# Optimization experiments

Hardware: AMD Instinct MI355X
Metric: run time of the kernel (lower is better)

## Reference

```python
import jax, jax.numpy as jnp
import numpy as np

N_NODES = 50000
N_EDGES = 100000
N_RELS = 64
D_IN = 64
D_OUT = 64


def setup_inputs() -> dict:
    key = jax.random.key(0)
    k1, k2, k3, k4, k5, k6 = jax.random.split(key, 6)
    h = jax.random.normal(k1, (N_NODES, D_IN), dtype=jnp.float32)
    src = jax.random.randint(k2, (N_EDGES,), 0, N_NODES)
    rel = jax.random.randint(k3, (N_EDGES,), 0, N_RELS)
    dst = jax.random.randint(k4, (N_EDGES,), 0, N_NODES)
    edges = jnp.stack([src, rel, dst], axis=1)
    # xavier_uniform with gain for relu: bound = gain * sqrt(6 / (fan_in + fan_out))
    gain = float(np.sqrt(2.0))
    bound = gain * float(np.sqrt(6.0 / (D_IN + D_OUT)))
    weight = jax.random.uniform(k5, (N_RELS, D_IN, D_OUT), dtype=jnp.float32,
                                minval=-bound, maxval=bound)
    self_loop_weight = jax.random.uniform(k6, (D_IN, D_OUT), dtype=jnp.float32,
                                          minval=-bound, maxval=bound)
    return {"h": h, "edges": edges, "weight": weight,
            "self_loop_weight": self_loop_weight}


def reference(h, edges, weight, self_loop_weight):
    # h: (N, D_IN); edges: (E, 3) int columns (src, rel, dst)
    src, rel, dst = edges[:, 0], edges[:, 1], edges[:, 2]
    n_nodes = h.shape[0]
    n_edges = src.shape[0]

    # per-edge relation-specific transform: (E,1,in) bmm (E,in,out) -> (E,out)
    src_h = h[src]                                    # (E, D_IN)
    msg = jnp.einsum('ei,eio->eo', src_h, weight[rel])  # (E, D_OUT)

    # -> last edge index per destination node
    last_edge = jax.ops.segment_max(jnp.arange(n_edges, dtype=jnp.int32), dst,
                                    num_segments=n_nodes)  # (N,)
    # msg = msg[index_matrix[dst]]: every edge to node d takes the msg of the
    # last edge pointing to d
    msg = msg[last_edge[dst]]                          # (E, D_OUT)

    # scatter-mean aggregate over dst (only nodes with incoming edges updated)
    sums = jax.ops.segment_sum(msg, dst, num_segments=n_nodes)          # (N, D_OUT)
    counts = jax.ops.segment_sum(jnp.ones((n_edges,), h.dtype), dst,
                                 num_segments=n_nodes)                   # (N,)
    has_in = counts > 0
    agg = jnp.where(has_in[:, None],
                    sums / jnp.maximum(counts, 1.0)[:, None], 0.0)

    out = h @ self_loop_weight                         # (N, D_OUT)
    return out + agg
```

## Files before the change

kernel.cpp:

```cpp
#include <hip/hip_runtime.h>

#define NN 50000
#define NE 100000
#define NREL 64
#define D 64
#define RCAP 1280
#define SCAP 8192
#define CSTR 16
#define BR   8
#define SBLK 64
#define FILL_BLOCKS 128
#define FILL_ITERS  2

typedef unsigned long long u64;
using f16x8 = __attribute__((ext_vector_type(8))) _Float16;
using f32x4 = __attribute__((ext_vector_type(4))) float;

#define WS_CURSOR  (400 * 1024)
#define WS_RBUCKET (408 * 1024)
#define WS_SBUCKET (736 * 1024)
#define WS_H2      (768 * 1024)
#define WS_WST     (7168 * 1024)
#define WS_W16T    (7176 * 1024)

struct H4 { _Float16 v[4]; };

__global__ __launch_bounds__(256) void k_pre(
    const float* __restrict__ h, const float* __restrict__ weight,
    const float* __restrict__ wself, u64* __restrict__ packed,
    int* __restrict__ cursor, _Float16* __restrict__ h2,
    _Float16* __restrict__ w16T, _Float16* __restrict__ wsT)
{
    const int t = blockIdx.x * 256 + threadIdx.x;
    const int nthr = gridDim.x * 256;
    for (int i = t; i < NN; i += nthr) packed[i] = 0ull;
    if (t < 65) cursor[t * CSTR] = 0;

    const float4* __restrict__ hf4 = reinterpret_cast<const float4*>(h);
    H4* __restrict__ o4 = reinterpret_cast<H4*>(h2);
    for (int m = t; m < NN * (D / 4); m += nthr) {
        const float4 p = hf4[m];
        H4 o;
        o.v[0] = (_Float16)p.x; o.v[1] = (_Float16)p.y;
        o.v[2] = (_Float16)p.z; o.v[3] = (_Float16)p.w;
        o4[m] = o;
    }

    const float4* __restrict__ W4 = reinterpret_cast<const float4*>(weight);
    for (int m = t; m < NREL * D * D / 4; m += nthr) {
        const float4 w = W4[m];
        const int r   = m >> 10;
        const int rem = m & 1023;
        const int k   = rem >> 4;
        const int n0  = (rem & 15) << 2;
        _Float16* __restrict__ base = w16T + ((size_t)r << 12) + k;
        base[(size_t)(n0 + 0) * D] = (_Float16)w.x;
        base[(size_t)(n0 + 1) * D] = (_Float16)w.y;
        base[(size_t)(n0 + 2) * D] = (_Float16)w.z;
        base[(size_t)(n0 + 3) * D] = (_Float16)w.w;
    }

    const float4* __restrict__ WS4 = reinterpret_cast<const float4*>(wself);
    for (int m = t; m < D * D / 4; m += nthr) {
        const float4 w = WS4[m];
        const int k  = m >> 4;
        const int n0 = (m & 15) << 2;
        wsT[(size_t)(n0 + 0) * D + k] = (_Float16)w.x;
        wsT[(size_t)(n0 + 1) * D + k] = (_Float16)w.y;
        wsT[(size_t)(n0 + 2) * D + k] = (_Float16)w.z;
        wsT[(size_t)(n0 + 3) * D + k] = (_Float16)w.w;
    }
}

__global__ void k_scatter(const int* __restrict__ edges, u64* __restrict__ packed) {
    int e = blockIdx.x * blockDim.x + threadIdx.x;
    if (e < NE) {
        int s = edges[e * 3 + 0];
        int r = edges[e * 3 + 1];
        int d = edges[e * 3 + 2];
        u64 key = ((u64)(e + 1) << 22) | ((u64)r << 16) | (u64)s;
        atomicMax(&packed[d], key);
    }
}

__global__ __launch_bounds__(256) void k_fill(
    const u64* __restrict__ packed, int* __restrict__ cursor,
    unsigned* __restrict__ rbucket, unsigned* __restrict__ sbucket)
{
    __shared__ int hcnt[65];
    __shared__ int hbase[65];
    const int t = threadIdx.x;
    if (t < 65) hcnt[t] = 0;
    __syncthreads();

    int      myr[FILL_ITERS];
    int      myslot[FILL_ITERS];
    unsigned myent[FILL_ITERS];

    #pragma unroll
    for (int it = 0; it < FILL_ITERS; ++it) {
        const int v = (blockIdx.x * FILL_ITERS + it) * 256 + t;
        myr[it] = -1;
        if (v < NN) {
            u64 key = packed[v];
            if (key) {
                myr[it]   = (int)((key >> 16) & 63);
                myent[it] = ((unsigned)v << 16) | (unsigned)(key & 0xFFFF);
            } else {
                myr[it]   = 64;
                myent[it] = (unsigned)v;
            }
            myslot[it] = atomicAdd(&hcnt[myr[it]], 1);
        }
    }
    __syncthreads();
    if (t < 65 && hcnt[t] > 0)
        hbase[t] = atomicAdd(&cursor[t * CSTR], hcnt[t]);
    __syncthreads();

    #pragma unroll
    for (int it = 0; it < FILL_ITERS; ++it) {
        const int r = myr[it];
        if (r >= 0) {
            const int p = hbase[r] + myslot[it];
            if (r < 64) { if (p < RCAP) rbucket[r * RCAP + p] = myent[it]; }
            else        { if (p < SCAP) sbucket[p] = myent[it]; }
        }
    }
}

__global__ __launch_bounds__(256) void k_compute(
    const _Float16* __restrict__ h2, const _Float16* __restrict__ w16T,
    const _Float16* __restrict__ wsT, const unsigned* __restrict__ rbucket,
    const unsigned* __restrict__ sbucket, const int* __restrict__ cursor,
    float* __restrict__ out)
{
    const int lane = threadIdx.x & 63;
    const int wv   = threadIdx.x >> 6;
    const bool isRel = blockIdx.x < NREL * BR;

    int r = 64, wslot, wstride, cnt;
    const unsigned* __restrict__ seg;
    if (isRel) {
        r = blockIdx.x / BR;
        wslot = (blockIdx.x % BR) * 4 + wv;
        wstride = BR * 4;
        seg = rbucket + r * RCAP;
        cnt = min(cursor[r * CSTR], RCAP);
    } else {
        wslot = (blockIdx.x - NREL * BR) * 4 + wv;
        wstride = SBLK * 4;
        seg = sbucket;
        cnt = min(cursor[64 * CSTR], SCAP);
    }
    if (cnt == 0 || wslot * 16 >= cnt) return;

    const int kbase = (lane >> 4) * 8;
    const int ncol  = lane & 15;

    f16x8 bws[4][2];
    #pragma unroll
    for (int nt = 0; nt < 4; ++nt)
        #pragma unroll
        for (int ks = 0; ks < 2; ++ks)
            bws[nt][ks] = *reinterpret_cast<const f16x8*>(
                wsT + (size_t)(nt * 16 + ncol) * D + ks * 32 + kbase);

    f16x8 bw[4][2];
    if (isRel) {
        const _Float16* __restrict__ wr = w16T + ((size_t)r << 12);
        #pragma unroll
        for (int nt = 0; nt < 4; ++nt)
            #pragma unroll
            for (int ks = 0; ks < 2; ++ks)
                bw[nt][ks] = *reinterpret_cast<const f16x8*>(
                    wr + (size_t)(nt * 16 + ncol) * D + ks * 32 + kbase);
    }

    for (int t = wslot; t * 16 < cnt; t += wstride) {
        const int myidx = min(t * 16 + ncol, cnt - 1);
        const unsigned ent = seg[myidx];
        const int v = isRel ? (int)(ent >> 16) : (int)ent;
        const int s = (int)(ent & 0xFFFF);

        f32x4 c[4];
        #pragma unroll
        for (int nt = 0; nt < 4; ++nt) c[nt] = (f32x4){0.f, 0.f, 0.f, 0.f};

        {
            const f16x8 a0 = *reinterpret_cast<const f16x8*>(h2 + (size_t)v * D + kbase);
            const f16x8 a1 = *reinterpret_cast<const f16x8*>(h2 + (size_t)v * D + 32 + kbase);
            #pragma unroll
            for (int nt = 0; nt < 4; ++nt) {
                c[nt] = __builtin_amdgcn_mfma_f32_16x16x32_f16(a0, bws[nt][0], c[nt], 0, 0, 0);
                c[nt] = __builtin_amdgcn_mfma_f32_16x16x32_f16(a1, bws[nt][1], c[nt], 0, 0, 0);
            }
        }
        if (isRel) {
            const f16x8 a0 = *reinterpret_cast<const f16x8*>(h2 + (size_t)s * D + kbase);
            const f16x8 a1 = *reinterpret_cast<const f16x8*>(h2 + (size_t)s * D + 32 + kbase);
            #pragma unroll
            for (int nt = 0; nt < 4; ++nt) {
                c[nt] = __builtin_amdgcn_mfma_f32_16x16x32_f16(a0, bw[nt][0], c[nt], 0, 0, 0);
                c[nt] = __builtin_amdgcn_mfma_f32_16x16x32_f16(a1, bw[nt][1], c[nt], 0, 0, 0);
            }
        }

        int vrow[4];
        #pragma unroll
        for (int q = 0; q < 4; ++q)
            vrow[q] = __shfl(v, (lane >> 4) * 4 + q, 64);

        #pragma unroll
        for (int nt = 0; nt < 4; ++nt)
            #pragma unroll
            for (int q = 0; q < 4; ++q)
                out[(size_t)vrow[q] * D + nt * 16 + ncol] = c[nt][q];
    }
}

extern "C" void kernel_launch(void* const* d_in, const int* in_sizes, int n_in,
                              void* d_out, int out_size, void* d_ws, size_t ws_size,
                              hipStream_t stream) {
    const float* h      = (const float*)d_in[0];
    const int*   edges  = (const int*)d_in[1];
    const float* weight = (const float*)d_in[2];
    const float* wself  = (const float*)d_in[3];
    float* out = (float*)d_out;

    char* ws = (char*)d_ws;
    u64*      packed  = (u64*)ws;
    int*      cursor  = (int*)(ws + WS_CURSOR);
    unsigned* rbucket = (unsigned*)(ws + WS_RBUCKET);
    unsigned* sbucket = (unsigned*)(ws + WS_SBUCKET);
    _Float16* h2      = (_Float16*)(ws + WS_H2);
    _Float16* wsT     = (_Float16*)(ws + WS_WST);
    _Float16* w16T    = (_Float16*)(ws + WS_W16T);

    k_pre<<<512, 256, 0, stream>>>(h, weight, wself, packed, cursor, h2, w16T, wsT);
    k_scatter<<<(NE + 255) / 256, 256, 0, stream>>>(edges, packed);
    k_fill<<<FILL_BLOCKS, 256, 0, stream>>>(packed, cursor, rbucket, sbucket);
    k_compute<<<NREL * BR + SBLK, 256, 0, stream>>>(h2, w16T, wsT, rbucket, sbucket, cursor, out);
}
```

Baseline: 33.73 us.

## Fuse edge scatter with preprocessing, transpose weights via LDS, swap MFMA operands for vector stores

Splits the zeroing into a small init kernel and merges the edge atomicMax scatter with the fp16 conversion of h and the weights into one heterogeneous kernel, with block ranges assigned per task. The weight transpose now goes through a shared-memory tile so the global writes are coalesced instead of strided. In the compute kernel the MFMA operands are swapped so each lane owns four contiguous output columns of its own row, allowing float4 stores without shuffles. The kernel count stays at four, but the heavy preprocessing now overlaps with the scatter.

```diff
diff --git a/kernel.cpp b/kernel.cpp
--- a/kernel.cpp
+++ b/kernel.cpp
@@ -12,6 +12,10 @@
 #define FILL_BLOCKS 128
 #define FILL_ITERS  2
 
+#define SC_BLK ((NE + 255) / 256)
+#define TR_BLK 65
+#define HC_BLK 160
+
 typedef unsigned long long u64;
 using f16x8 = __attribute__((ext_vector_type(8))) _Float16;
 using f32x4 = __attribute__((ext_vector_type(4))) float;
@@ -25,17 +29,60 @@
 
 struct H4 { _Float16 v[4]; };
 
-__global__ __launch_bounds__(256) void k_pre(
-    const float* __restrict__ h, const float* __restrict__ weight,
-    const float* __restrict__ wself, u64* __restrict__ packed,
-    int* __restrict__ cursor, _Float16* __restrict__ h2,
-    _Float16* __restrict__ w16T, _Float16* __restrict__ wsT)
-{
+__global__ __launch_bounds__(256) void k_init(u64* __restrict__ packed, int* __restrict__ cursor) {
     const int t = blockIdx.x * 256 + threadIdx.x;
     const int nthr = gridDim.x * 256;
     for (int i = t; i < NN; i += nthr) packed[i] = 0ull;
     if (t < 65) cursor[t * CSTR] = 0;
-
+}
+
+__global__ __launch_bounds__(256) void k_scatpre(
+    const int* __restrict__ edges, const float* __restrict__ h,
+    const float* __restrict__ weight, const float* __restrict__ wself,
+    u64* __restrict__ packed, _Float16* __restrict__ h2,
+    _Float16* __restrict__ w16T, _Float16* __restrict__ wsT)
+{
+    __shared__ _Float16 tile[D * D];
+
+    if (blockIdx.x < SC_BLK) {
+        const int e = blockIdx.x * 256 + threadIdx.x;
+        if (e < NE) {
+            const int s = edges[e * 3 + 0];
+            const int r = edges[e * 3 + 1];
+            const int d = edges[e * 3 + 2];
+            const u64 key = ((u64)(e + 1) << 22) | ((u64)r << 16) | (u64)s;
+            atomicMax(&packed[d], key);
+        }
+        return;
+    }
+
+    if (blockIdx.x < SC_BLK + TR_BLK) {
+        const int r = blockIdx.x - SC_BLK;
+        const float4* __restrict__ src4 = reinterpret_cast<const float4*>(
+            (r < NREL) ? (weight + (size_t)r * D * D) : wself);
+        #pragma unroll
+        for (int it = 0; it < 4; ++it) {
+            const int idx = it * 256 + threadIdx.x;
+            const float4 w = src4[idx];
+            const int k  = idx >> 4;
+            const int n0 = (idx & 15) << 2;
+            tile[(n0 + 0) * D + k] = (_Float16)w.x;
+            tile[(n0 + 1) * D + k] = (_Float16)w.y;
+            tile[(n0 + 2) * D + k] = (_Float16)w.z;
+            tile[(n0 + 3) * D + k] = (_Float16)w.w;
+        }
+        __syncthreads();
+        f16x8* __restrict__ dst = reinterpret_cast<f16x8*>(
+            (r < NREL) ? (w16T + ((size_t)r << 12)) : wsT);
+        const f16x8* __restrict__ src = reinterpret_cast<const f16x8*>(tile);
+        #pragma unroll
+        for (int it = 0; it < 2; ++it)
+            dst[it * 256 + threadIdx.x] = src[it * 256 + threadIdx.x];
+        return;
+    }
+
+    const int t = (blockIdx.x - SC_BLK - TR_BLK) * 256 + threadIdx.x;
+    const int nthr = HC_BLK * 256;
     const float4* __restrict__ hf4 = reinterpret_cast<const float4*>(h);
     H4* __restrict__ o4 = reinterpret_cast<H4*>(h2);
     for (int m = t; m < NN * (D / 4); m += nthr) {
@@ -44,42 +91,6 @@
         o.v[0] = (_Float16)p.x; o.v[1] = (_Float16)p.y;
         o.v[2] = (_Float16)p.z; o.v[3] = (_Float16)p.w;
         o4[m] = o;
-    }
-
-    const float4* __restrict__ W4 = reinterpret_cast<const float4*>(weight);
-    for (int m = t; m < NREL * D * D / 4; m += nthr) {
-        const float4 w = W4[m];
-        const int r   = m >> 10;
-        const int rem = m & 1023;
-        const int k   = rem >> 4;
-        const int n0  = (rem & 15) << 2;
-        _Float16* __restrict__ base = w16T + ((size_t)r << 12) + k;
-        base[(size_t)(n0 + 0) * D] = (_Float16)w.x;
-        base[(size_t)(n0 + 1) * D] = (_Float16)w.y;
-        base[(size_t)(n0 + 2) * D] = (_Float16)w.z;
-        base[(size_t)(n0 + 3) * D] = (_Float16)w.w;
-    }
-
-    const float4* __restrict__ WS4 = reinterpret_cast<const float4*>(wself);
-    for (int m = t; m < D * D / 4; m += nthr) {
-        const float4 w = WS4[m];
-        const int k  = m >> 4;
-        const int n0 = (m & 15) << 2;
-        wsT[(size_t)(n0 + 0) * D + k] = (_Float16)w.x;
-        wsT[(size_t)(n0 + 1) * D + k] = (_Float16)w.y;
-        wsT[(size_t)(n0 + 2) * D + k] = (_Float16)w.z;
-        wsT[(size_t)(n0 + 3) * D + k] = (_Float16)w.w;
-    }
-}
-
-__global__ void k_scatter(const int* __restrict__ edges, u64* __restrict__ packed) {
-    int e = blockIdx.x * blockDim.x + threadIdx.x;
-    if (e < NE) {
-        int s = edges[e * 3 + 0];
-        int r = edges[e * 3 + 1];
-        int d = edges[e * 3 + 2];
-        u64 key = ((u64)(e + 1) << 22) | ((u64)r << 16) | (u64)s;
-        atomicMax(&packed[d], key);
     }
 }
 
@@ -158,28 +169,27 @@
     const int kbase = (lane >> 4) * 8;
     const int ncol  = lane & 15;
 
-    f16x8 bws[4][2];
+    f16x8 was[4][2];
     #pragma unroll
     for (int nt = 0; nt < 4; ++nt)
         #pragma unroll
         for (int ks = 0; ks < 2; ++ks)
-            bws[nt][ks] = *reinterpret_cast<const f16x8*>(
+            was[nt][ks] = *reinterpret_cast<const f16x8*>(
                 wsT + (size_t)(nt * 16 + ncol) * D + ks * 32 + kbase);
 
-    f16x8 bw[4][2];
+    f16x8 wa[4][2];
     if (isRel) {
         const _Float16* __restrict__ wr = w16T + ((size_t)r << 12);
         #pragma unroll
         for (int nt = 0; nt < 4; ++nt)
             #pragma unroll
             for (int ks = 0; ks < 2; ++ks)
-                bw[nt][ks] = *reinterpret_cast<const f16x8*>(
+                wa[nt][ks] = *reinterpret_cast<const f16x8*>(
                     wr + (size_t)(nt * 16 + ncol) * D + ks * 32 + kbase);
     }
 
     for (int t = wslot; t * 16 < cnt; t += wstride) {
-        const int myidx = min(t * 16 + ncol, cnt - 1);
-        const unsigned ent = seg[myidx];
+        const unsigned ent = seg[min(t * 16 + ncol, cnt - 1)];
         const int v = isRel ? (int)(ent >> 16) : (int)ent;
         const int s = (int)(ent & 0xFFFF);
 
@@ -188,34 +198,30 @@
         for (int nt = 0; nt < 4; ++nt) c[nt] = (f32x4){0.f, 0.f, 0.f, 0.f};
 
         {
-            const f16x8 a0 = *reinterpret_cast<const f16x8*>(h2 + (size_t)v * D + kbase);
-            const f16x8 a1 = *reinterpret_cast<const f16x8*>(h2 + (size_t)v * D + 32 + kbase);
+            const f16x8 b0 = *reinterpret_cast<const f16x8*>(h2 + (size_t)v * D + kbase);
+            const f16x8 b1 = *reinterpret_cast<const f16x8*>(h2 + (size_t)v * D + 32 + kbase);
             #pragma unroll
             for (int nt = 0; nt < 4; ++nt) {
-                c[nt] = __builtin_amdgcn_mfma_f32_16x16x32_f16(a0, bws[nt][0], c[nt], 0, 0, 0);
-                c[nt] = __builtin_amdgcn_mfma_f32_16x16x32_f16(a1, bws[nt][1], c[nt], 0, 0, 0);
+                c[nt] = __builtin_amdgcn_mfma_f32_16x16x32_f16(was[nt][0], b0, c[nt], 0, 0, 0);
+                c[nt] = __builtin_amdgcn_mfma_f32_16x16x32_f16(was[nt][1], b1, c[nt], 0, 0, 0);
             }
         }
         if (isRel) {
-            const f16x8 a0 = *reinterpret_cast<const f16x8*>(h2 + (size_t)s * D + kbase);
-            const f16x8 a1 = *reinterpret_cast<const f16x8*>(h2 + (size_t)s * D + 32 + kbase);
+            const f16x8 b0 = *reinterpret_cast<const f16x8*>(h2 + (size_t)s * D + kbase);
+            const f16x8 b1 = *reinterpret_cast<const f16x8*>(h2 + (size_t)s * D + 32 + kbase);
             #pragma unroll
             for (int nt = 0; nt < 4; ++nt) {
-                c[nt] = __builtin_amdgcn_mfma_f32_16x16x32_f16(a0, bw[nt][0], c[nt], 0, 0, 0);
-                c[nt] = __builtin_amdgcn_mfma_f32_16x16x32_f16(a1, bw[nt][1], c[nt], 0, 0, 0);
+                c[nt] = __builtin_amdgcn_mfma_f32_16x16x32_f16(wa[nt][0], b0, c[nt], 0, 0, 0);
+                c[nt] = __builtin_amdgcn_mfma_f32_16x16x32_f16(wa[nt][1], b1, c[nt], 0, 0, 0);
             }
         }
 
-        int vrow[4];
-        #pragma unroll
-        for (int q = 0; q < 4; ++q)
-            vrow[q] = __shfl(v, (lane >> 4) * 4 + q, 64);
-
-        #pragma unroll
-        for (int nt = 0; nt < 4; ++nt)
-            #pragma unroll
-            for (int q = 0; q < 4; ++q)
-                out[(size_t)vrow[q] * D + nt * 16 + ncol] = c[nt][q];
+        float* __restrict__ orow = out + (size_t)v * D + (lane >> 4) * 4;
+        #pragma unroll
+        for (int nt = 0; nt < 4; ++nt) {
+            *reinterpret_cast<float4*>(orow + nt * 16) =
+                make_float4(c[nt][0], c[nt][1], c[nt][2], c[nt][3]);
+        }
     }
 }
 
@@ -237,8 +243,9 @@
     _Float16* wsT     = (_Float16*)(ws + WS_WST);
     _Float16* w16T    = (_Float16*)(ws + WS_W16T);
 
-    k_pre<<<512, 256, 0, stream>>>(h, weight, wself, packed, cursor, h2, w16T, wsT);
-    k_scatter<<<(NE + 255) / 256, 256, 0, stream>>>(edges, packed);
+    k_init<<<98, 256, 0, stream>>>(packed, cursor);
+    k_scatpre<<<SC_BLK + TR_BLK + HC_BLK, 256, 0, stream>>>(
+        edges, h, weight, wself, packed, h2, w16T, wsT);
     k_fill<<<FILL_BLOCKS, 256, 0, stream>>>(packed, cursor, rbucket, sbucket);
     k_compute<<<NREL * BR + SBLK, 256, 0, stream>>>(h2, w16T, wsT, rbucket, sbucket, cursor, out);
 }
```

Result: slower. 39.94 us (+18.4%).
